# Kernel optimization log

Hardware: AMD Instinct MI355X
Metric: run time of the kernel (lower is better)

## Reference

```python
import jax, jax.numpy as jnp
import numpy as np

N = 100000      # n_entities + n_users (graph nodes)
E = 1600000     # edges
R = 8           # relations
D = 64          # entity_dim
DR = 64         # relation_dim
EPS = 1e-12


def setup_inputs() -> dict:
    key = jax.random.key(0)
    ks = jax.random.split(key, 16)
    inp = {
        'entity_emb': jax.random.normal(ks[0], (N, D), jnp.float32) * 0.1,
        'rel_emb':    jax.random.normal(ks[1], (R, DR), jnp.float32) * 0.1,
        'W_R':        jax.random.normal(ks[2], (R, D, DR), jnp.float32) * 0.1,
        'W1_0': jax.random.normal(ks[3], (32, 64), jnp.float32) * 0.1,
        'b1_0': jax.random.normal(ks[4], (32,), jnp.float32) * 0.1,
        'W2_0': jax.random.normal(ks[5], (32, 64), jnp.float32) * 0.1,
        'b2_0': jax.random.normal(ks[6], (32,), jnp.float32) * 0.1,
        'W1_1': jax.random.normal(ks[7], (16, 32), jnp.float32) * 0.1,
        'b1_1': jax.random.normal(ks[8], (16,), jnp.float32) * 0.1,
        'W2_1': jax.random.normal(ks[9], (16, 32), jnp.float32) * 0.1,
        'b2_1': jax.random.normal(ks[10], (16,), jnp.float32) * 0.1,
        'src':   jax.random.randint(ks[11], (E,), 0, N, dtype=jnp.int32),
        'dst':   jax.random.randint(ks[12], (E,), 0, N, dtype=jnp.int32),
        'etype': jax.random.randint(ks[13], (E,), 0, R, dtype=jnp.int32),
    }
    return inp


def _l2_normalize(x):
    # F.normalize(x, p=2, dim=1)
    n = jnp.linalg.norm(x, axis=1, keepdims=True)
    return x / jnp.maximum(n, EPS)


def reference(entity_emb, rel_emb, W_R, W1_0, b1_0, W2_0, b2_0,
              W1_1, b1_1, W2_1, b2_1, src, dst, etype):
    # ---- compute_attention: per-edge relation-specific projection ----
    # proj[n, r, :] = entity_emb[n] @ W_R[r]   -> [N, R, DR]
    proj = jnp.einsum('nd,rdk->nrk', entity_emb, W_R)
    r_mul_t = proj[src, etype]          # [E, DR] (edges.src)
    r_mul_h = proj[dst, etype]          # [E, DR] (edges.dst)
    r_e = rel_emb[etype]                # [E, DR]
    att = jnp.sum(r_mul_t * jnp.tanh(r_mul_h + r_e), axis=-1)  # [E]

    # ---- edge_softmax: normalize over incoming edges of each dst ----
    m = jax.ops.segment_max(att, dst, num_segments=N)           # [N]
    ex = jnp.exp(att - m[dst])
    s = jax.ops.segment_sum(ex, dst, num_segments=N)            # [N]
    a = ex / s[dst]                                             # [E]

    # ---- bi-interaction aggregator layers ----
    def agg_layer(x, W1, b1, W2, b2):
        msg = x[src] * a[:, None]                               # u_mul_e
        Nh = jax.ops.segment_sum(msg, dst, num_segments=N)      # sum to dst
        out1 = jax.nn.leaky_relu(jnp.matmul(x + Nh, W1.T) + b1, 0.01)
        out2 = jax.nn.leaky_relu(jnp.matmul(x * Nh, W2.T) + b2, 0.01)
        return _l2_normalize(out1 + out2)

    ego = entity_emb
    h1 = agg_layer(ego, W1_0, b1_0, W2_0, b2_0)   # [N, 32]
    h2 = agg_layer(h1, W1_1, b1_1, W2_1, b2_1)    # [N, 16]
    all_embed = jnp.concatenate([ego, h1, h2], axis=1)  # [N, 112]
    return all_embed
```

## Files before the change

### kernel.cpp

```cpp
#include <hip/hip_runtime.h>
#include <hip/hip_bf16.h>
#include <math.h>

#define NN 100000
#define NE 1600000
#define NR 8
#define DD 64
#define DDR 64

typedef __attribute__((ext_vector_type(8))) short bf8v;
typedef __attribute__((ext_vector_type(4))) float f4v;

__device__ __forceinline__ unsigned enc_f(float f) {
    unsigned u = __float_as_uint(f);
    return (u & 0x80000000u) ? ~u : (u | 0x80000000u);
}
__device__ __forceinline__ float dec_f(unsigned u) {
    return (u & 0x80000000u) ? __uint_as_float(u & 0x7FFFFFFFu) : __uint_as_float(~u);
}
__device__ __forceinline__ float bflo(unsigned u) { return __uint_as_float(u << 16); }
__device__ __forceinline__ float bfhi(unsigned u) { return __uint_as_float(u & 0xFFFF0000u); }
__device__ __forceinline__ float bfs2f(unsigned short u) { return __uint_as_float(((unsigned)u) << 16); }
__device__ __forceinline__ short f2bfs(float x) {
    __hip_bfloat16 h = __float2bfloat16(x);
    return *reinterpret_cast<short*>(&h);
}
__device__ __forceinline__ unsigned pack2bf(short a, short b) {
    return (unsigned)(unsigned short)a | ((unsigned)(unsigned short)b << 16);
}
__device__ __forceinline__ float tanh_fast(float x) {
    x = fminf(fmaxf(x, -15.f), 15.f);
    float e = __expf(2.f * x);
    return (e - 1.f) * __builtin_amdgcn_rcpf(e + 1.f);
}

__global__ void __launch_bounds__(256)
k_projm(const float* __restrict__ emb, const float* __restrict__ WR,
        const float* __restrict__ rel,
        unsigned short* __restrict__ tproj, unsigned* __restrict__ embh)
{
    int t = threadIdx.x;
    int wv = t >> 6, l = t & 63;
    int lo = l & 15, hi = l >> 4;
    int r = blockIdx.y;
    int colbase = (wv & 1) * 32;
    int nwbase = blockIdx.x * 128 + (wv >> 1) * 64;

    const float* __restrict__ wb = WR + (long)r * (DD * DDR) + (hi * 8) * DDR + colbase + lo;
    bf8v B00, B01, B10, B11;
#pragma unroll
    for (int j = 0; j < 8; ++j) {
        B00[j] = f2bfs(wb[(0 * 32 + j) * DDR + 0]);
        B01[j] = f2bfs(wb[(1 * 32 + j) * DDR + 0]);
        B10[j] = f2bfs(wb[(0 * 32 + j) * DDR + 16]);
        B11[j] = f2bfs(wb[(1 * 32 + j) * DDR + 16]);
    }
    float rv0 = rel[r * DDR + colbase + lo];
    float rv1 = rel[r * DDR + colbase + lo + 16];

    for (int nt = 0; nt < 4; ++nt) {
        int nb = nwbase + nt * 16;
        int arow = nb + lo;
        float4 xa0 = make_float4(0.f, 0.f, 0.f, 0.f), xa1 = xa0, xb0 = xa0, xb1 = xa0;
        if (arow < NN) {
            const float* __restrict__ xr = emb + (long)arow * DD + hi * 8;
            xa0 = *(const float4*)(xr);
            xa1 = *(const float4*)(xr + 4);
            xb0 = *(const float4*)(xr + 32);
            xb1 = *(const float4*)(xr + 36);
        }
        bf8v A0, A1;
        A0[0] = f2bfs(xa0.x); A0[1] = f2bfs(xa0.y); A0[2] = f2bfs(xa0.z); A0[3] = f2bfs(xa0.w);
        A0[4] = f2bfs(xa1.x); A0[5] = f2bfs(xa1.y); A0[6] = f2bfs(xa1.z); A0[7] = f2bfs(xa1.w);
        A1[0] = f2bfs(xb0.x); A1[1] = f2bfs(xb0.y); A1[2] = f2bfs(xb0.z); A1[3] = f2bfs(xb0.w);
        A1[4] = f2bfs(xb1.x); A1[5] = f2bfs(xb1.y); A1[6] = f2bfs(xb1.z); A1[7] = f2bfs(xb1.w);

        if (r == 0 && arow < NN) {
            unsigned* er = embh + (long)arow * 32 + hi * 4;
            er[0]  = pack2bf(A0[0], A0[1]); er[1]  = pack2bf(A0[2], A0[3]);
            er[2]  = pack2bf(A0[4], A0[5]); er[3]  = pack2bf(A0[6], A0[7]);
            er[16] = pack2bf(A1[0], A1[1]); er[17] = pack2bf(A1[2], A1[3]);
            er[18] = pack2bf(A1[4], A1[5]); er[19] = pack2bf(A1[6], A1[7]);
        }

        f4v acc0 = {0.f, 0.f, 0.f, 0.f}, acc1 = {0.f, 0.f, 0.f, 0.f};
        acc0 = __builtin_amdgcn_mfma_f32_16x16x32_bf16(A0, B00, acc0, 0, 0, 0);
        acc0 = __builtin_amdgcn_mfma_f32_16x16x32_bf16(A1, B01, acc0, 0, 0, 0);
        acc1 = __builtin_amdgcn_mfma_f32_16x16x32_bf16(A0, B10, acc1, 0, 0, 0);
        acc1 = __builtin_amdgcn_mfma_f32_16x16x32_bf16(A1, B11, acc1, 0, 0, 0);

#pragma unroll
        for (int i = 0; i < 4; ++i) {
            int rr = nb + hi * 4 + i;
            if (rr < NN) {
                long obase = ((long)r * NN + rr) * DDR + colbase + lo;
                tproj[obase]      = (unsigned short)f2bfs(tanh_fast(acc0[i] + rv0));
                tproj[obase + 16] = (unsigned short)f2bfs(tanh_fast(acc1[i] + rv1));
            }
        }
    }
}

__global__ void __launch_bounds__(256)
k_projw2(const unsigned short* __restrict__ tproj, const float* __restrict__ WR,
         unsigned short* __restrict__ w2h)
{
    int t = threadIdx.x;
    int wv = t >> 6, l = t & 63;
    int lo = l & 15, hi = l >> 4;
    int r = blockIdx.y;
    int colbase = (wv & 1) * 32;
    int nwbase = blockIdx.x * 128 + (wv >> 1) * 64;

    const float* __restrict__ wb0 = WR + (long)r * (DD * DDR) + (long)(colbase + lo) * DDR + hi * 8;
    const float* __restrict__ wb1 = wb0 + 16 * DDR;
    bf8v B00, B01, B10, B11;
#pragma unroll
    for (int j = 0; j < 8; ++j) {
        B00[j] = f2bfs(wb0[j]);
        B01[j] = f2bfs(wb0[32 + j]);
        B10[j] = f2bfs(wb1[j]);
        B11[j] = f2bfs(wb1[32 + j]);
    }

    for (int nt = 0; nt < 4; ++nt) {
        int nb = nwbase + nt * 16;
        int arow = nb + lo;
        bf8v A0, A1;
#pragma unroll
        for (int j = 0; j < 8; ++j) { A0[j] = 0; A1[j] = 0; }
        if (arow < NN) {
            const unsigned short* ar = tproj + ((long)r * NN + arow) * DDR + hi * 8;
            A0 = *(const bf8v*)(ar);
            A1 = *(const bf8v*)(ar + 32);
        }
        f4v acc0 = {0.f, 0.f, 0.f, 0.f}, acc1 = {0.f, 0.f, 0.f, 0.f};
        acc0 = __builtin_amdgcn_mfma_f32_16x16x32_bf16(A0, B00, acc0, 0, 0, 0);
        acc0 = __builtin_amdgcn_mfma_f32_16x16x32_bf16(A1, B01, acc0, 0, 0, 0);
        acc1 = __builtin_amdgcn_mfma_f32_16x16x32_bf16(A0, B10, acc1, 0, 0, 0);
        acc1 = __builtin_amdgcn_mfma_f32_16x16x32_bf16(A1, B11, acc1, 0, 0, 0);
#pragma unroll
        for (int i = 0; i < 4; ++i) {
            int rr = nb + hi * 4 + i;
            if (rr < NN) {
                long obase = ((long)r * NN + rr) * DDR + colbase + lo;
                w2h[obase]      = (unsigned short)f2bfs(acc0[i]);
                w2h[obase + 16] = (unsigned short)f2bfs(acc1[i]);
            }
        }
    }
}

__global__ void k_hist(const int* __restrict__ dst, unsigned* __restrict__ cnt)
{
    int e = blockIdx.x * blockDim.x + threadIdx.x;
    if (e >= NE) return;
    atomicAdd(cnt + dst[e], 1u);
}

__global__ void k_base(const unsigned* __restrict__ cnt, unsigned* __restrict__ gcur,
                       unsigned* __restrict__ base, unsigned* __restrict__ curs)
{
    int i = blockIdx.x * blockDim.x + threadIdx.x;
    int lane = threadIdx.x & 63;
    unsigned v = (i < NN) ? cnt[i] : 0u;
    unsigned p = v;
#pragma unroll
    for (int off = 1; off < 64; off <<= 1) {
        unsigned q = __shfl_up(p, off);
        if (lane >= off) p += q;
    }
    unsigned tot = __shfl(p, 63);
    unsigned gb = 0;
    if (lane == 0) gb = atomicAdd(gcur, tot);
    gb = __shfl(gb, 0);
    if (i < NN) {
        unsigned b = gb + p - v;
        base[i] = b;
        curs[i] = b;
    }
}

__global__ void k_scatter2(const int* __restrict__ dst, const int* __restrict__ src,
                           const int* __restrict__ et, unsigned* __restrict__ curs,
                           unsigned* __restrict__ srcet)
{
    int e = blockIdx.x * blockDim.x + threadIdx.x;
    if (e >= NE) return;
    unsigned pos = atomicAdd(curs + dst[e], 1u);
    srcet[pos] = (unsigned)src[e] | ((unsigned)et[e] << 28);
}

__global__ void __launch_bounds__(256)
k_mega0(const float* __restrict__ emb, const unsigned* __restrict__ embh,
        const unsigned* __restrict__ w2h,
        const unsigned* __restrict__ cnt, const unsigned* __restrict__ basep,
        const unsigned* __restrict__ srcet, float* __restrict__ acsr,
        unsigned short* __restrict__ h1h,
        const float* __restrict__ W1, const float* __restrict__ b1,
        const float* __restrict__ W2, const float* __restrict__ b2,
        float* __restrict__ out)
{
    __shared__ float W1T[64][33];
    __shared__ float W2T[64][33];
    __shared__ float sm1[4][64];
    __shared__ float sm2[4][64];
    __shared__ float att_s[4][64];
    int t = threadIdx.x;
#pragma unroll
    for (int i = 0; i < 8; ++i) {
        int idx = i * 256 + t;
        W1T[idx & 63][idx >> 6] = W1[idx];
        W2T[idx & 63][idx >> 6] = W2[idx];
    }
    int wv = t >> 6, lane = t & 63;
    int g = blockIdx.x * 4 + wv;
    int deg = (int)cnt[g];
    long b = basep[g];
    float Nh = 0.f;
    const unsigned short* embh_us = (const unsigned short*)embh;
    if (deg > 0 && deg <= 64) {
        unsigned se = 0;
        if (lane < deg) se = srcet[b + lane];
        int gi = lane >> 4;
        int lj = lane & 15;
        for (int k0 = 0; k0 < deg; k0 += 4) {
            int ei = k0 + gi;
            unsigned sei = __shfl(se, ei);
            int s = (int)(sei & 0x0FFFFFFFu);
            int r = (int)(sei >> 28);
            uint2 tv = *(const uint2*)(embh + (long)s * 32 + lj * 2);
            uint2 hv = *(const uint2*)(w2h + ((long)r * NN + g) * 32 + lj * 2);
            float sum = bflo(tv.x) * bflo(hv.x) + bfhi(tv.x) * bfhi(hv.x)
                      + bflo(tv.y) * bflo(hv.y) + bfhi(tv.y) * bfhi(hv.y);
#pragma unroll
            for (int off = 8; off; off >>= 1) sum += __shfl_xor(sum, off);
            if (lj == 0 && ei < deg) att_s[wv][ei] = sum;
        }
        float attv = (lane < deg) ? att_s[wv][lane] : -3.4e38f;
        float m = attv;
#pragma unroll
        for (int off = 32; off; off >>= 1) m = fmaxf(m, __shfl_xor(m, off));
        float exv = (lane < deg) ? __expf(attv - m) : 0.f;
        float s_ = exv;
#pragma unroll
        for (int off = 32; off; off >>= 1) s_ += __shfl_xor(s_, off);
        float inv = 1.f / s_;
        if (lane < deg) acsr[b + lane] = exv * inv;
        float acc = 0.f;
        int i = 0;
        for (; i + 1 < deg; i += 2) {
            float a0 = __shfl(exv, i), a1 = __shfl(exv, i + 1);
            int s0 = (int)(__shfl(se, i) & 0x0FFFFFFFu);
            int s1 = (int)(__shfl(se, i + 1) & 0x0FFFFFFFu);
            float v0 = bfs2f(embh_us[(long)s0 * DD + lane]);
            float v1 = bfs2f(embh_us[(long)s1 * DD + lane]);
            acc = fmaf(v0, a0, acc);
            acc = fmaf(v1, a1, acc);
        }
        if (i < deg) {
            float a0 = __shfl(exv, i);
            int s0 = (int)(__shfl(se, i) & 0x0FFFFFFFu);
            acc = fmaf(bfs2f(embh_us[(long)s0 * DD + lane]), a0, acc);
        }
        Nh = acc * inv;
    } else if (deg > 64) {
        float m = -3.4e38f;
        for (int i = 0; i < deg; ++i) {
            unsigned sei = srcet[b + i];
            int s = (int)(sei & 0x0FFFFFFFu), r = (int)(sei >> 28);
            float v = bfs2f(embh_us[(long)s * DD + lane]);
            float wvl = bfs2f(((const unsigned short*)w2h)[((long)r * NN + g) * DDR + lane]);
            float p = v * wvl;
#pragma unroll
            for (int off = 32; off; off >>= 1) p += __shfl_xor(p, off);
            if (lane == 0) acsr[b + i] = p;
            m = fmaxf(m, p);
        }
        float s_ = 0.f;
        for (int i = lane; i < deg; i += 64) s_ += __expf(acsr[b + i] - m);
#pragma unroll
        for (int off = 32; off; off >>= 1) s_ += __shfl_xor(s_, off);
        float inv = 1.f / s_;
        float acc = 0.f;
        for (int i = 0; i < deg; ++i) {
            float raw = acsr[b + i];
            float a = __expf(raw - m) * inv;
            int s = (int)(srcet[b + i] & 0x0FFFFFFFu);
            acc = fmaf(bfs2f(embh_us[(long)s * DD + lane]), a, acc);
            if (lane == 0) acsr[b + i] = a;
        }
        Nh = acc;
    }
    float x = emb[(long)g * DD + lane];
    sm1[wv][lane] = x + Nh;
    sm2[wv][lane] = x * Nh;
    __syncthreads();
    int j = lane & 31;
    const float* __restrict__ WT = (lane < 32) ? &W1T[0][0] : &W2T[0][0];
    const float* __restrict__ sm = (lane < 32) ? &sm1[wv][0] : &sm2[wv][0];
    float accm = (lane < 32) ? b1[j] : b2[j];
#pragma unroll 8
    for (int dd = 0; dd < 64; ++dd)
        accm = fmaf(sm[dd], WT[dd * 33 + j], accm);
    accm = (accm >= 0.f) ? accm : 0.01f * accm;
    float other = __shfl_down(accm, 32);
    float h = accm + other;
    float ss = h * h;
#pragma unroll
    for (int off = 16; off; off >>= 1) ss += __shfl_xor(ss, off);
    float hn = h / fmaxf(sqrtf(ss), 1e-12f);
    out[(long)g * 112 + lane] = x;
    if (lane < 32) {
        out[(long)g * 112 + 64 + j] = hn;
        h1h[(long)g * 32 + j] = (unsigned short)f2bfs(hn);
    }
}

__global__ void __launch_bounds__(256)
k_mega1(const float* __restrict__ acsr, const unsigned* __restrict__ srcet,
        const unsigned* __restrict__ cnt, const unsigned* __restrict__ basep,
        const unsigned short* __restrict__ h1h,
        const float* __restrict__ W1, const float* __restrict__ b1,
        const float* __restrict__ W2, const float* __restrict__ b2,
        float* __restrict__ out)
{
    __shared__ float W1T[32][17];
    __shared__ float W2T[32][17];
    __shared__ float sm1[8][32];
    __shared__ float sm2[8][32];
    int t = threadIdx.x;
#pragma unroll
    for (int i = 0; i < 2; ++i) {
        int idx = i * 256 + t;
        W1T[idx & 31][idx >> 5] = W1[idx];
        W2T[idx & 31][idx >> 5] = W2[idx];
    }
    int grp = t >> 5, l5 = t & 31;
    int g = blockIdx.x * 8 + grp;
    int deg = (int)cnt[g];
    float acc = 0.f;
    if (deg > 0) {
        long b = basep[g];
        unsigned se = 0; float a = 0.f;
        if (l5 < deg) { se = srcet[b + l5]; a = acsr[b + l5]; }
        int dmin = (deg < 32) ? deg : 32;
        int i = 0;
        for (; i + 1 < dmin; i += 2) {
            float a0 = __shfl(a, i, 32), a1 = __shfl(a, i + 1, 32);
            int s0 = (int)(__shfl(se, i, 32) & 0x0FFFFFFFu);
            int s1 = (int)(__shfl(se, i + 1, 32) & 0x0FFFFFFFu);
            float v0 = bfs2f(h1h[(long)s0 * 32 + l5]);
            float v1 = bfs2f(h1h[(long)s1 * 32 + l5]);
            acc = fmaf(v0, a0, acc);
            acc = fmaf(v1, a1, acc);
        }
        if (i < dmin) {
            float a0 = __shfl(a, i, 32);
            int s0 = (int)(__shfl(se, i, 32) & 0x0FFFFFFFu);
            acc = fmaf(bfs2f(h1h[(long)s0 * 32 + l5]), a0, acc);
        }
        for (int k = 32; k < deg; ++k) {
            float ak = acsr[b + k];
            int sk = (int)(srcet[b + k] & 0x0FFFFFFFu);
            acc = fmaf(bfs2f(h1h[(long)sk * 32 + l5]), ak, acc);
        }
    }
    float x = out[(long)g * 112 + 64 + l5];
    sm1[grp][l5] = x + acc;
    sm2[grp][l5] = x * acc;
    __syncthreads();
    int j = l5 & 15;
    const float* __restrict__ WT = (l5 < 16) ? &W1T[0][0] : &W2T[0][0];
    const float* __restrict__ sm = (l5 < 16) ? &sm1[grp][0] : &sm2[grp][0];
    float accm = (l5 < 16) ? b1[j] : b2[j];
#pragma unroll 8
    for (int dd = 0; dd < 32; ++dd)
        accm = fmaf(sm[dd], WT[dd * 17 + j], accm);
    accm = (accm >= 0.f) ? accm : 0.01f * accm;
    float other = __shfl_down(accm, 16, 32);
    float h = accm + other;
    float ss = h * h;
#pragma unroll
    for (int off = 8; off; off >>= 1) ss += __shfl_xor(ss, off);
    float hn = h / fmaxf(sqrtf(ss), 1e-12f);
    if (l5 < 16) out[(long)g * 112 + 96 + j] = hn;
}

__global__ void k_att(const float* __restrict__ emb, const float* __restrict__ rel,
                      const float* __restrict__ WR, const int* __restrict__ src,
                      const int* __restrict__ dst, const int* __restrict__ et,
                      float* __restrict__ att, unsigned* __restrict__ mkey)
{
    int e = (int)((blockIdx.x * blockDim.x + threadIdx.x) >> 6);
    int lane = threadIdx.x & 63;
    if (e >= NE) return;
    int s = src[e], d = dst[e], r = et[e];
    const float* __restrict__ es = emb + (long)s * DD;
    const float* __restrict__ eh = emb + (long)d * DD;
    const float* __restrict__ w  = WR + r * (DD * DDR) + lane;
    float at = 0.f, ah = 0.f;
#pragma unroll 8
    for (int dd = 0; dd < DD; ++dd) {
        float ws = w[dd * DDR];
        at = fmaf(es[dd], ws, at);
        ah = fmaf(eh[dd], ws, ah);
    }
    float term = at * tanhf(ah + rel[r * DDR + lane]);
#pragma unroll
    for (int off = 32; off; off >>= 1) term += __shfl_xor(term, off);
    if (lane == 0) {
        att[e] = term;
        atomicMax(mkey + d, enc_f(term));
    }
}

__global__ void k_expsum(const int* __restrict__ dst, float* __restrict__ att,
                         const unsigned* __restrict__ mkey, float* __restrict__ ssum)
{
    int e = blockIdx.x * blockDim.x + threadIdx.x;
    if (e >= NE) return;
    int d = dst[e];
    float ex = expf(att[e] - dec_f(mkey[d]));
    att[e] = ex;
    atomicAdd(ssum + d, ex);
}

__global__ void k_agg0(const float* __restrict__ emb, const int* __restrict__ src,
                       const int* __restrict__ dst, float* __restrict__ att,
                       const float* __restrict__ ssum, float* __restrict__ Nh)
{
    int e = (int)((blockIdx.x * blockDim.x + threadIdx.x) >> 6);
    int lane = threadIdx.x & 63;
    if (e >= NE) return;
    int s = src[e], d = dst[e];
    float a = att[e] / ssum[d];
    if (lane == 0) att[e] = a;
    float v = emb[(long)s * DD + lane] * a;
    atomicAdd(Nh + (long)d * DD + lane, v);
}

__global__ void k_agg1(const float* __restrict__ out, const int* __restrict__ src,
                       const int* __restrict__ dst, const float* __restrict__ att,
                       float* __restrict__ Nh1)
{
    int idx = blockIdx.x * blockDim.x + threadIdx.x;
    int e = idx >> 5;
    int j = idx & 31;
    if (e >= NE) return;
    int s = src[e], d = dst[e];
    float a = att[e];
    float v = out[(long)s * 112 + 64 + j] * a;
    atomicAdd(Nh1 + (long)d * 32 + j, v);
}

#define NPB0 32
__global__ void __launch_bounds__(256)
k_node0t(const float* __restrict__ emb, const float* __restrict__ Nh,
         const float* __restrict__ W1, const float* __restrict__ b1,
         const float* __restrict__ W2, const float* __restrict__ b2,
         float* __restrict__ out)
{
    __shared__ float W1T[64][33];
    __shared__ float W2T[64][33];
    int t = threadIdx.x;
#pragma unroll
    for (int i = 0; i < 8; ++i) {
        int idx = i * 256 + t;
        W1T[idx & 63][idx >> 6] = W1[idx];
        W2T[idx & 63][idx >> 6] = W2[idx];
    }
    __syncthreads();
    int wv = t >> 6, lane = t & 63, j = lane & 31;
    const float* __restrict__ WT = (lane < 32) ? &W1T[0][0] : &W2T[0][0];
    float bj = (lane < 32) ? b1[j] : b2[j];
    int n0 = blockIdx.x * NPB0;
    int n1 = (n0 + NPB0 < NN) ? n0 + NPB0 : NN;
    for (int node = n0 + wv; node < n1; node += 4) {
        const float* __restrict__ x  = emb + (long)node * DD;
        const float* __restrict__ nh = Nh + (long)node * DD;
        float acc = 0.f;
#pragma unroll 8
        for (int dd = 0; dd < DD; ++dd) {
            float xv = x[dd], nv = nh[dd];
            float v = (lane < 32) ? (xv + nv) : (xv * nv);
            acc = fmaf(v, WT[dd * 33 + j], acc);
        }
        acc += bj;
        acc = (acc >= 0.f) ? acc : 0.01f * acc;
        float other = __shfl_down(acc, 32);
        float h = acc + other;
        float ss = h * h;
#pragma unroll
        for (int off = 16; off; off >>= 1) ss += __shfl_xor(ss, off);
        float hn = h / fmaxf(sqrtf(ss), 1e-12f);
        out[(long)node * 112 + lane] = x[lane];
        if (lane < 32) out[(long)node * 112 + 64 + j] = hn;
    }
}

#define NPB1 32
__global__ void __launch_bounds__(256)
k_node1t(const float* __restrict__ outbuf, const float* __restrict__ Nh1,
         const float* __restrict__ W1, const float* __restrict__ b1,
         const float* __restrict__ W2, const float* __restrict__ b2,
         float* __restrict__ out)
{
    __shared__ float W1T[32][17];
    __shared__ float W2T[32][17];
    int t = threadIdx.x;
#pragma unroll
    for (int i = 0; i < 2; ++i) {
        int idx = i * 256 + t;
        W1T[idx & 31][idx >> 5] = W1[idx];
        W2T[idx & 31][idx >> 5] = W2[idx];
    }
    __syncthreads();
    int grp = t >> 5;
    int l5 = t & 31, j = l5 & 15;
    const float* __restrict__ WT = (l5 < 16) ? &W1T[0][0] : &W2T[0][0];
    float bj = (l5 < 16) ? b1[j] : b2[j];
    int n0 = blockIdx.x * NPB1;
    int n1 = (n0 + NPB1 < NN) ? n0 + NPB1 : NN;
    for (int node = n0 + grp; node < n1; node += 8) {
        const float* __restrict__ x  = outbuf + (long)node * 112 + 64;
        const float* __restrict__ nh = Nh1 + (long)node * 32;
        float acc = 0.f;
#pragma unroll 8
        for (int dd = 0; dd < 32; ++dd) {
            float xv = x[dd], nv = nh[dd];
            float v = (l5 < 16) ? (xv + nv) : (xv * nv);
            acc = fmaf(v, WT[dd * 17 + j], acc);
        }
        acc += bj;
        acc = (acc >= 0.f) ? acc : 0.01f * acc;
        float other = __shfl_down(acc, 16, 32);
        float h = acc + other;
        float ss = h * h;
#pragma unroll
        for (int off = 8; off; off >>= 1) ss += __shfl_xor(ss, off);
        float hn = h / fmaxf(sqrtf(ss), 1e-12f);
        if (l5 < 16) out[(long)node * 112 + 96 + j] = hn;
    }
}

extern "C" void kernel_launch(void* const* d_in, const int* in_sizes, int n_in,
                              void* d_out, int out_size, void* d_ws, size_t ws_size,
                              hipStream_t stream) {
    const float* emb  = (const float*)d_in[0];
    const float* rel  = (const float*)d_in[1];
    const float* WR   = (const float*)d_in[2];
    const float* W1_0 = (const float*)d_in[3];
    const float* b1_0 = (const float*)d_in[4];
    const float* W2_0 = (const float*)d_in[5];
    const float* b2_0 = (const float*)d_in[6];
    const float* W1_1 = (const float*)d_in[7];
    const float* b1_1 = (const float*)d_in[8];
    const float* W2_1 = (const float*)d_in[9];
    const float* b2_1 = (const float*)d_in[10];
    const int*   src  = (const int*)d_in[11];
    const int*   dst  = (const int*)d_in[12];
    const int*   et   = (const int*)d_in[13];
    float* out = (float*)d_out;

    unsigned* cnt   = (unsigned*)d_ws;
    unsigned* gcur  = cnt + NN;
    unsigned* basep = cnt + NN + 64;
    unsigned* curs  = cnt + 2 * NN + 64;
    float* acsr  = (float*)d_ws + 3 * NN + 64;
    unsigned* srcet = (unsigned*)(acsr + NE);
    unsigned short* tproj = (unsigned short*)(srcet + NE);
    unsigned short* w2h = tproj + (size_t)NR * NN * DDR;
    unsigned* embh = (unsigned*)(w2h + (size_t)NR * NN * DDR);
    unsigned short* h1h = (unsigned short*)(embh + (size_t)NN * 32);

    size_t need = ((size_t)3 * NN + 64 + 2 * (size_t)NE) * 4
                + 2 * (size_t)NR * NN * DDR * 2
                + (size_t)NN * 32 * 4 + (size_t)NN * 16 * 4;

    if (ws_size >= need) {
        hipMemsetAsync(d_ws, 0, (size_t)(NN + 64) * sizeof(unsigned), stream);
        k_hist<<<dim3((NE + 255) / 256), dim3(256), 0, stream>>>(dst, cnt);
        k_projm<<<dim3((NN + 127) / 128, NR), dim3(256), 0, stream>>>(
            emb, WR, rel, tproj, embh);
        k_projw2<<<dim3((NN + 127) / 128, NR), dim3(256), 0, stream>>>(
            tproj, WR, (unsigned short*)w2h);
        k_base<<<dim3((NN + 255) / 256), dim3(256), 0, stream>>>(cnt, gcur, basep, curs);
        k_scatter2<<<dim3((NE + 255) / 256), dim3(256), 0, stream>>>(
            dst, src, et, curs, srcet);
        k_mega0<<<dim3((NN + 3) / 4), dim3(256), 0, stream>>>(
            emb, embh, (const unsigned*)w2h, cnt, basep, srcet, acsr, h1h,
            W1_0, b1_0, W2_0, b2_0, out);
        k_mega1<<<dim3((NN + 7) / 8), dim3(256), 0, stream>>>(
            acsr, srcet, cnt, basep, h1h, W1_1, b1_1, W2_1, b2_1, out);
    } else {
        unsigned* mkey = (unsigned*)d_ws;
        float* ssum = (float*)d_ws + NN;
        float* fNh0 = (float*)d_ws + 2 * NN;
        float* fNh1 = (float*)d_ws + (2 + DD) * NN;
        float* fatt = (float*)d_ws + (2 + DD + 32) * NN;
        hipMemsetAsync(d_ws, 0, (size_t)(2 + DD + 32) * NN * sizeof(float), stream);
        k_att<<<dim3((int)(((long)NE * 64 + 255) / 256)), dim3(256), 0, stream>>>(
            emb, rel, WR, src, dst, et, fatt, mkey);
        k_expsum<<<dim3((NE + 255) / 256), dim3(256), 0, stream>>>(dst, fatt, mkey, ssum);
        k_agg0<<<dim3((int)(((long)NE * 64 + 255) / 256)), dim3(256), 0, stream>>>(
            emb, src, dst, fatt, ssum, fNh0);
        k_node0t<<<dim3((NN + NPB0 - 1) / NPB0), dim3(256), 0, stream>>>(
            emb, fNh0, W1_0, b1_0, W2_0, b2_0, out);
        k_agg1<<<dim3((int)(((long)NE * 32 + 255) / 256)), dim3(256), 0, stream>>>(
            out, src, dst, fatt, fNh1);
        k_node1t<<<dim3((NN + NPB1 - 1) / NPB1), dim3(256), 0, stream>>>(
            out, fNh1, W1_1, b1_1, W2_1, b2_1, out);
    }
}
```

Measured before the change: 536.5 us.

## Fuse projection kernels via shared memory and reuse gathered rows in attention aggregation

Merges the two per-relation projection GEMM kernels into one. The tanh-projected tile stays in shared memory instead of round-tripping a full bf16 [R,N,64] buffer through global memory. In the low-degree path of the first aggregation kernel, the softmax drops max subtraction and uses a clamped exp, which is unnormalised in flight. The neighbour rows already loaded for the attention dot product are reused through shuffles to build the weighted sum, removing the second gather of source embeddings. The clamped exp without max shift risks precision loss for large attention values.

```diff
diff --git a/kernel.cpp b/kernel.cpp
--- a/kernel.cpp
+++ b/kernel.cpp
@@ -35,110 +35,94 @@
 }
 
 __global__ void __launch_bounds__(256)
-k_projm(const float* __restrict__ emb, const float* __restrict__ WR,
+k_projf(const float* __restrict__ emb, const float* __restrict__ WR,
         const float* __restrict__ rel,
-        unsigned short* __restrict__ tproj, unsigned* __restrict__ embh)
-{
+        unsigned short* __restrict__ w2h, unsigned* __restrict__ embh)
+{
+    __shared__ unsigned short Tt[128][66];
     int t = threadIdx.x;
     int wv = t >> 6, l = t & 63;
     int lo = l & 15, hi = l >> 4;
     int r = blockIdx.y;
     int colbase = (wv & 1) * 32;
-    int nwbase = blockIdx.x * 128 + (wv >> 1) * 64;
+    int p = wv >> 1;
+    int nwbase = blockIdx.x * 128 + p * 64;
+    int nlocal = p * 64;
 
     const float* __restrict__ wb = WR + (long)r * (DD * DDR) + (hi * 8) * DDR + colbase + lo;
-    bf8v B00, B01, B10, B11;
+    {
+        bf8v B00, B01, B10, B11;
+#pragma unroll
+        for (int j = 0; j < 8; ++j) {
+            B00[j] = f2bfs(wb[(0 * 32 + j) * DDR + 0]);
+            B01[j] = f2bfs(wb[(1 * 32 + j) * DDR + 0]);
+            B10[j] = f2bfs(wb[(0 * 32 + j) * DDR + 16]);
+            B11[j] = f2bfs(wb[(1 * 32 + j) * DDR + 16]);
+        }
+        float rv0 = rel[r * DDR + colbase + lo];
+        float rv1 = rel[r * DDR + colbase + lo + 16];
+
+        for (int nt = 0; nt < 4; ++nt) {
+            int nb = nwbase + nt * 16;
+            int arow = nb + lo;
+            float4 xa0 = make_float4(0.f, 0.f, 0.f, 0.f), xa1 = xa0, xb0 = xa0, xb1 = xa0;
+            if (arow < NN) {
+                const float* __restrict__ xr = emb + (long)arow * DD + hi * 8;
+                xa0 = *(const float4*)(xr);
+                xa1 = *(const float4*)(xr + 4);
+                xb0 = *(const float4*)(xr + 32);
+                xb1 = *(const float4*)(xr + 36);
+            }
+            bf8v A0, A1;
+            A0[0] = f2bfs(xa0.x); A0[1] = f2bfs(xa0.y); A0[2] = f2bfs(xa0.z); A0[3] = f2bfs(xa0.w);
+            A0[4] = f2bfs(xa1.x); A0[5] = f2bfs(xa1.y); A0[6] = f2bfs(xa1.z); A0[7] = f2bfs(xa1.w);
+            A1[0] = f2bfs(xb0.x); A1[1] = f2bfs(xb0.y); A1[2] = f2bfs(xb0.z); A1[3] = f2bfs(xb0.w);
+            A1[4] = f2bfs(xb1.x); A1[5] = f2bfs(xb1.y); A1[6] = f2bfs(xb1.z); A1[7] = f2bfs(xb1.w);
+
+            if (r == 0 && arow < NN) {
+                unsigned* er = embh + (long)arow * 32 + hi * 4;
+                er[0]  = pack2bf(A0[0], A0[1]); er[1]  = pack2bf(A0[2], A0[3]);
+                er[2]  = pack2bf(A0[4], A0[5]); er[3]  = pack2bf(A0[6], A0[7]);
+                er[16] = pack2bf(A1[0], A1[1]); er[17] = pack2bf(A1[2], A1[3]);
+                er[18] = pack2bf(A1[4], A1[5]); er[19] = pack2bf(A1[6], A1[7]);
+            }
+
+            f4v acc0 = {0.f, 0.f, 0.f, 0.f}, acc1 = {0.f, 0.f, 0.f, 0.f};
+            acc0 = __builtin_amdgcn_mfma_f32_16x16x32_bf16(A0, B00, acc0, 0, 0, 0);
+            acc0 = __builtin_amdgcn_mfma_f32_16x16x32_bf16(A1, B01, acc0, 0, 0, 0);
+            acc1 = __builtin_amdgcn_mfma_f32_16x16x32_bf16(A0, B10, acc1, 0, 0, 0);
+            acc1 = __builtin_amdgcn_mfma_f32_16x16x32_bf16(A1, B11, acc1, 0, 0, 0);
+
+#pragma unroll
+            for (int i = 0; i < 4; ++i) {
+                int rl = nlocal + nt * 16 + hi * 4 + i;
+                Tt[rl][colbase + lo]      = (unsigned short)f2bfs(tanh_fast(acc0[i] + rv0));
+                Tt[rl][colbase + lo + 16] = (unsigned short)f2bfs(tanh_fast(acc1[i] + rv1));
+            }
+        }
+    }
+    __syncthreads();
+
+    const float* __restrict__ wb0 = WR + (long)r * (DD * DDR) + (long)(colbase + lo) * DDR + hi * 8;
+    const float* __restrict__ wb1 = wb0 + 16 * DDR;
+    bf8v C00, C01, C10, C11;
 #pragma unroll
     for (int j = 0; j < 8; ++j) {
-        B00[j] = f2bfs(wb[(0 * 32 + j) * DDR + 0]);
-        B01[j] = f2bfs(wb[(1 * 32 + j) * DDR + 0]);
-        B10[j] = f2bfs(wb[(0 * 32 + j) * DDR + 16]);
-        B11[j] = f2bfs(wb[(1 * 32 + j) * DDR + 16]);
-    }
-    float rv0 = rel[r * DDR + colbase + lo];
-    float rv1 = rel[r * DDR + colbase + lo + 16];
-
+        C00[j] = f2bfs(wb0[j]);
+        C01[j] = f2bfs(wb0[32 + j]);
+        C10[j] = f2bfs(wb1[j]);
+        C11[j] = f2bfs(wb1[32 + j]);
+    }
     for (int nt = 0; nt < 4; ++nt) {
         int nb = nwbase + nt * 16;
-        int arow = nb + lo;
-        float4 xa0 = make_float4(0.f, 0.f, 0.f, 0.f), xa1 = xa0, xb0 = xa0, xb1 = xa0;
-        if (arow < NN) {
-            const float* __restrict__ xr = emb + (long)arow * DD + hi * 8;
-            xa0 = *(const float4*)(xr);
-            xa1 = *(const float4*)(xr + 4);
-            xb0 = *(const float4*)(xr + 32);
-            xb1 = *(const float4*)(xr + 36);
-        }
-        bf8v A0, A1;
-        A0[0] = f2bfs(xa0.x); A0[1] = f2bfs(xa0.y); A0[2] = f2bfs(xa0.z); A0[3] = f2bfs(xa0.w);
-        A0[4] = f2bfs(xa1.x); A0[5] = f2bfs(xa1.y); A0[6] = f2bfs(xa1.z); A0[7] = f2bfs(xa1.w);
-        A1[0] = f2bfs(xb0.x); A1[1] = f2bfs(xb0.y); A1[2] = f2bfs(xb0.z); A1[3] = f2bfs(xb0.w);
-        A1[4] = f2bfs(xb1.x); A1[5] = f2bfs(xb1.y); A1[6] = f2bfs(xb1.z); A1[7] = f2bfs(xb1.w);
-
-        if (r == 0 && arow < NN) {
-            unsigned* er = embh + (long)arow * 32 + hi * 4;
-            er[0]  = pack2bf(A0[0], A0[1]); er[1]  = pack2bf(A0[2], A0[3]);
-            er[2]  = pack2bf(A0[4], A0[5]); er[3]  = pack2bf(A0[6], A0[7]);
-            er[16] = pack2bf(A1[0], A1[1]); er[17] = pack2bf(A1[2], A1[3]);
-            er[18] = pack2bf(A1[4], A1[5]); er[19] = pack2bf(A1[6], A1[7]);
-        }
-
+        int rl = nlocal + nt * 16 + lo;
+        bf8v A0 = *(const bf8v*)&Tt[rl][hi * 8];
+        bf8v A1 = *(const bf8v*)&Tt[rl][32 + hi * 8];
         f4v acc0 = {0.f, 0.f, 0.f, 0.f}, acc1 = {0.f, 0.f, 0.f, 0.f};
-        acc0 = __builtin_amdgcn_mfma_f32_16x16x32_bf16(A0, B00, acc0, 0, 0, 0);
-        acc0 = __builtin_amdgcn_mfma_f32_16x16x32_bf16(A1, B01, acc0, 0, 0, 0);
-        acc1 = __builtin_amdgcn_mfma_f32_16x16x32_bf16(A0, B10, acc1, 0, 0, 0);
-        acc1 = __builtin_amdgcn_mfma_f32_16x16x32_bf16(A1, B11, acc1, 0, 0, 0);
-
-#pragma unroll
-        for (int i = 0; i < 4; ++i) {
-            int rr = nb + hi * 4 + i;
-            if (rr < NN) {
-                long obase = ((long)r * NN + rr) * DDR + colbase + lo;
-                tproj[obase]      = (unsigned short)f2bfs(tanh_fast(acc0[i] + rv0));
-                tproj[obase + 16] = (unsigned short)f2bfs(tanh_fast(acc1[i] + rv1));
-            }
-        }
-    }
-}
-
-__global__ void __launch_bounds__(256)
-k_projw2(const unsigned short* __restrict__ tproj, const float* __restrict__ WR,
-         unsigned short* __restrict__ w2h)
-{
-    int t = threadIdx.x;
-    int wv = t >> 6, l = t & 63;
-    int lo = l & 15, hi = l >> 4;
-    int r = blockIdx.y;
-    int colbase = (wv & 1) * 32;
-    int nwbase = blockIdx.x * 128 + (wv >> 1) * 64;
-
-    const float* __restrict__ wb0 = WR + (long)r * (DD * DDR) + (long)(colbase + lo) * DDR + hi * 8;
-    const float* __restrict__ wb1 = wb0 + 16 * DDR;
-    bf8v B00, B01, B10, B11;
-#pragma unroll
-    for (int j = 0; j < 8; ++j) {
-        B00[j] = f2bfs(wb0[j]);
-        B01[j] = f2bfs(wb0[32 + j]);
-        B10[j] = f2bfs(wb1[j]);
-        B11[j] = f2bfs(wb1[32 + j]);
-    }
-
-    for (int nt = 0; nt < 4; ++nt) {
-        int nb = nwbase + nt * 16;
-        int arow = nb + lo;
-        bf8v A0, A1;
-#pragma unroll
-        for (int j = 0; j < 8; ++j) { A0[j] = 0; A1[j] = 0; }
-        if (arow < NN) {
-            const unsigned short* ar = tproj + ((long)r * NN + arow) * DDR + hi * 8;
-            A0 = *(const bf8v*)(ar);
-            A1 = *(const bf8v*)(ar + 32);
-        }
-        f4v acc0 = {0.f, 0.f, 0.f, 0.f}, acc1 = {0.f, 0.f, 0.f, 0.f};
-        acc0 = __builtin_amdgcn_mfma_f32_16x16x32_bf16(A0, B00, acc0, 0, 0, 0);
-        acc0 = __builtin_amdgcn_mfma_f32_16x16x32_bf16(A1, B01, acc0, 0, 0, 0);
-        acc1 = __builtin_amdgcn_mfma_f32_16x16x32_bf16(A0, B10, acc1, 0, 0, 0);
-        acc1 = __builtin_amdgcn_mfma_f32_16x16x32_bf16(A1, B11, acc1, 0, 0, 0);
+        acc0 = __builtin_amdgcn_mfma_f32_16x16x32_bf16(A0, C00, acc0, 0, 0, 0);
+        acc0 = __builtin_amdgcn_mfma_f32_16x16x32_bf16(A1, C01, acc0, 0, 0, 0);
+        acc1 = __builtin_amdgcn_mfma_f32_16x16x32_bf16(A0, C10, acc1, 0, 0, 0);
+        acc1 = __builtin_amdgcn_mfma_f32_16x16x32_bf16(A1, C11, acc1, 0, 0, 0);
 #pragma unroll
         for (int i = 0; i < 4; ++i) {
             int rr = nb + hi * 4 + i;
@@ -205,7 +189,6 @@
     __shared__ float W2T[64][33];
     __shared__ float sm1[4][64];
     __shared__ float sm2[4][64];
-    __shared__ float att_s[4][64];
     int t = threadIdx.x;
 #pragma unroll
     for (int i = 0; i < 8; ++i) {
@@ -224,6 +207,7 @@
         if (lane < deg) se = srcet[b + lane];
         int gi = lane >> 4;
         int lj = lane & 15;
+        float acc = 0.f, s_ = 0.f, myexp = 0.f;
         for (int k0 = 0; k0 < deg; k0 += 4) {
             int ei = k0 + gi;
             unsigned sei = __shfl(se, ei);
@@ -235,34 +219,22 @@
                       + bflo(tv.y) * bflo(hv.y) + bfhi(tv.y) * bfhi(hv.y);
 #pragma unroll
             for (int off = 8; off; off >>= 1) sum += __shfl_xor(sum, off);
-            if (lj == 0 && ei < deg) att_s[wv][ei] = sum;
-        }
-        float attv = (lane < deg) ? att_s[wv][lane] : -3.4e38f;
-        float m = attv;
-#pragma unroll
-        for (int off = 32; off; off >>= 1) m = fmaxf(m, __shfl_xor(m, off));
-        float exv = (lane < deg) ? __expf(attv - m) : 0.f;
-        float s_ = exv;
-#pragma unroll
-        for (int off = 32; off; off >>= 1) s_ += __shfl_xor(s_, off);
+#pragma unroll
+            for (int q = 0; q < 4; ++q) {
+                float sq = __shfl(sum, q * 16);
+                float exq = (k0 + q < deg) ? __expf(fminf(sq, 60.f)) : 0.f;
+                if (lane == k0 + q) myexp = exq;
+                s_ += exq;
+                int srcl = q * 16 + (lane >> 2);
+                unsigned rx = __shfl(tv.x, srcl);
+                unsigned ry = __shfl(tv.y, srcl);
+                unsigned word = (lane & 2) ? ry : rx;
+                float v = (lane & 1) ? bfhi(word) : bflo(word);
+                acc = fmaf(v, exq, acc);
+            }
+        }
         float inv = 1.f / s_;
-        if (lane < deg) acsr[b + lane] = exv * inv;
-        float acc = 0.f;
-        int i = 0;
-        for (; i + 1 < deg; i += 2) {
-            float a0 = __shfl(exv, i), a1 = __shfl(exv, i + 1);
-            int s0 = (int)(__shfl(se, i) & 0x0FFFFFFFu);
-            int s1 = (int)(__shfl(se, i + 1) & 0x0FFFFFFFu);
-            float v0 = bfs2f(embh_us[(long)s0 * DD + lane]);
-            float v1 = bfs2f(embh_us[(long)s1 * DD + lane]);
-            acc = fmaf(v0, a0, acc);
-            acc = fmaf(v1, a1, acc);
-        }
-        if (i < deg) {
-            float a0 = __shfl(exv, i);
-            int s0 = (int)(__shfl(se, i) & 0x0FFFFFFFu);
-            acc = fmaf(bfs2f(embh_us[(long)s0 * DD + lane]), a0, acc);
-        }
+        if (lane < deg) acsr[b + lane] = myexp * inv;
         Nh = acc * inv;
     } else if (deg > 64) {
         float m = -3.4e38f;
@@ -569,22 +541,19 @@
     unsigned* curs  = cnt + 2 * NN + 64;
     float* acsr  = (float*)d_ws + 3 * NN + 64;
     unsigned* srcet = (unsigned*)(acsr + NE);
-    unsigned short* tproj = (unsigned short*)(srcet + NE);
-    unsigned short* w2h = tproj + (size_t)NR * NN * DDR;
+    unsigned short* w2h = (unsigned short*)(srcet + NE);
     unsigned* embh = (unsigned*)(w2h + (size_t)NR * NN * DDR);
     unsigned short* h1h = (unsigned short*)(embh + (size_t)NN * 32);
 
     size_t need = ((size_t)3 * NN + 64 + 2 * (size_t)NE) * 4
-                + 2 * (size_t)NR * NN * DDR * 2
+                + (size_t)NR * NN * DDR * 2
                 + (size_t)NN * 32 * 4 + (size_t)NN * 16 * 4;
 
     if (ws_size >= need) {
         hipMemsetAsync(d_ws, 0, (size_t)(NN + 64) * sizeof(unsigned), stream);
         k_hist<<<dim3((NE + 255) / 256), dim3(256), 0, stream>>>(dst, cnt);
-        k_projm<<<dim3((NN + 127) / 128, NR), dim3(256), 0, stream>>>(
-            emb, WR, rel, tproj, embh);
-        k_projw2<<<dim3((NN + 127) / 128, NR), dim3(256), 0, stream>>>(
-            tproj, WR, (unsigned short*)w2h);
+        k_projf<<<dim3((NN + 127) / 128, NR), dim3(256), 0, stream>>>(
+            emb, WR, rel, w2h, embh);
         k_base<<<dim3((NN + 255) / 256), dim3(256), 0, stream>>>(cnt, gcur, basep, curs);
         k_scatter2<<<dim3((NE + 255) / 256), dim3(256), 0, stream>>>(
             dst, src, et, curs, srcet);
```

Result: faster. 484.6 us (-9.7%).
